# Optimization experiments

Measured on AMD Instinct MI355X. Metric: run time of the kernel, lower is better.

Reference implementation:

```python
import jax, jax.numpy as jnp
import numpy as np

N, E = 25000, 400000
IN, HID, OUT = 128, 256, 128
T = 4                      # towers
F1, F2 = HID // T, OUT // T  # per-tower out dims (divide_input=False)
A = 12                     # len(aggregators)=4 * len(scalers)=3
EPS_STD = 1e-5
EPS_BN = 1e-5


def _glorot(k, shape):
    fin, fout = shape[-2], shape[-1]
    lim = float(np.sqrt(6.0 / (fin + fout)))
    return jax.random.uniform(k, shape, jnp.float32, -lim, lim)


def setup_inputs():
    key = jax.random.key(0)
    ks = jax.random.split(key, 10)
    x = jax.random.normal(ks[0], (N, IN), jnp.float32)
    edge_index = jax.random.randint(ks[1], (2, E), 0, N, dtype=jnp.int32)
    # avg_deg['log'] buffer of PNAConv: mean over nodes of log(deg+1)
    deg = jax.ops.segment_sum(jnp.ones((E,), jnp.float32), edge_index[1], num_segments=N)
    avg_log = jnp.mean(jnp.log(deg + 1.0)).astype(jnp.float32)
    return dict(
        x=x, edge_index=edge_index, avg_log=avg_log,
        pre1_W=_glorot(ks[2], (T, 2 * IN, F1)), pre1_b=jnp.zeros((T, F1), jnp.float32),
        post1_W=_glorot(ks[3], (T, IN + A * F1, F1)), post1_b=jnp.zeros((T, F1), jnp.float32),
        lin1_W=_glorot(ks[4], (T * F1, HID)), lin1_b=jnp.zeros((HID,), jnp.float32),
        bn1_g=jnp.ones((HID,), jnp.float32), bn1_b=jnp.zeros((HID,), jnp.float32),
        pre2_W=_glorot(ks[5], (T, 2 * HID, F2)), pre2_b=jnp.zeros((T, F2), jnp.float32),
        post2_W=_glorot(ks[6], (T, HID + A * F2, F2)), post2_b=jnp.zeros((T, F2), jnp.float32),
        lin2_W=_glorot(ks[7], (T * F2, OUT)), lin2_b=jnp.zeros((OUT,), jnp.float32),
        bn2_g=jnp.ones((OUT,), jnp.float32), bn2_b=jnp.zeros((OUT,), jnp.float32),
    )


def _pna(x, src, tgt, preW, preB, postW, postB, linW, linB, avg_log):
    """PNAConv: towers=T, divide_input=False, pre_layers=post_layers=1,
    aggregators [mean,min,max,std], scalers [identity,amplification,attenuation]."""
    n = x.shape[0]
    # message: per tower Linear on concat([x_i, x_j]) where i=target, j=source
    h = jnp.concatenate([x[tgt], x[src]], axis=-1)            # [E, 2*F_in]
    msg = jnp.einsum('ec,tcf->etf', h, preW) + preB           # [E, T, F]
    ones = jnp.ones((msg.shape[0],), msg.dtype)
    deg = jax.ops.segment_sum(ones, tgt, num_segments=n)      # in-degree [n]
    degc = jnp.maximum(deg, 1.0)[:, None, None]
    s1 = jax.ops.segment_sum(msg, tgt, num_segments=n)
    mean = s1 / degc
    s2 = jax.ops.segment_sum(msg * msg, tgt, num_segments=n)
    var = jnp.maximum(s2 / degc - mean * mean, 0.0)
    std = jnp.sqrt(var + EPS_STD)
    has = (deg > 0.0)[:, None, None]
    mn = jnp.where(has, jax.ops.segment_min(msg, tgt, num_segments=n), 0.0)
    mx = jnp.where(has, jax.ops.segment_max(msg, tgt, num_segments=n), 0.0)
    agg = jnp.concatenate([mean, mn, mx, std], axis=-1)       # [n, T, 4F]
    dlog = jnp.log(jnp.maximum(deg, 1.0) + 1.0)[:, None, None]
    out = jnp.concatenate([agg, agg * (dlog / avg_log), agg * (avg_log / dlog)], axis=-1)  # [n, T, 12F]
    xt = jnp.broadcast_to(x[:, None, :], (n, T, x.shape[-1]))
    post_in = jnp.concatenate([xt, out], axis=-1)             # [n, T, F_in + 12F]
    post = jnp.einsum('ntc,tcf->ntf', post_in, postW) + postB # [n, T, F]
    return post.reshape(n, -1) @ linW + linB                  # [n, out]


def _bn(x, g, b):
    # BatchNorm1d training-mode math: biased batch variance
    m = jnp.mean(x, axis=0)
    v = jnp.mean((x - m) ** 2, axis=0)
    return g * (x - m) / jnp.sqrt(v + EPS_BN) + b


def reference(x, edge_index, avg_log, pre1_W, pre1_b, post1_W, post1_b, lin1_W, lin1_b,
              bn1_g, bn1_b, pre2_W, pre2_b, post2_W, post2_b, lin2_W, lin2_b, bn2_g, bn2_b):
    src, tgt = edge_index[0], edge_index[1]
    h = _pna(x, src, tgt, pre1_W, pre1_b, post1_W, post1_b, lin1_W, lin1_b, avg_log)
    h = jax.nn.relu(_bn(jnp.nan_to_num(h), bn1_g, bn1_b))
    h = _pna(h, src, tgt, pre2_W, pre2_b, post2_W, post2_b, lin2_W, lin2_b, avg_log)
    h = jax.nn.relu(_bn(jnp.nan_to_num(h), bn2_g, bn2_b))
    return h
```

## Files before the change

kernel.cpp:

```cpp
#include <hip/hip_runtime.h>
#include <hip/hip_bf16.h>
#include <float.h>
#include <math.h>

typedef __hip_bfloat16 bf16;
typedef __attribute__((ext_vector_type(8))) short short8;
typedef __attribute__((ext_vector_type(4))) float f32x4;

__device__ __forceinline__ float bf2f(bf16 v){ return __bfloat162float(v); }
__device__ __forceinline__ void stv(float* p, float v){ *p = v; }
__device__ __forceinline__ void stv(bf16* p, float v){ *p = __float2bfloat16(v); }
__device__ __forceinline__ float nanfix(float v){
  if (v != v) return 0.f;
  return fminf(fmaxf(v, -FLT_MAX), FLT_MAX);
}
__device__ __forceinline__ unsigned short f2bu(float f){
  unsigned u = __float_as_uint(f);
  unsigned r = u + 0x7FFFu + ((u>>16)&1u);
  return (unsigned short)(r>>16);
}
template<int VEC>
__device__ __forceinline__ void ldbf(const bf16* p, float (&o)[VEC]){
  if constexpr (VEC==4){
    ushort4 r = *(const ushort4*)p;
    o[0]=__uint_as_float((unsigned)r.x<<16); o[1]=__uint_as_float((unsigned)r.y<<16);
    o[2]=__uint_as_float((unsigned)r.z<<16); o[3]=__uint_as_float((unsigned)r.w<<16);
  } else {
    ushort2 r = *(const ushort2*)p;
    o[0]=__uint_as_float((unsigned)r.x<<16); o[1]=__uint_as_float((unsigned)r.y<<16);
  }
}

__device__ __forceinline__ void gl_lds16(const bf16* g, bf16* l){
  __builtin_amdgcn_global_load_lds(
      (const __attribute__((address_space(1))) void*)g,
      (__attribute__((address_space(3))) void*)l, 16, 0, 0);
}

__global__ void k_scan1(const int* __restrict__ deg, int* __restrict__ bsum, int N){
  __shared__ int sm[256];
  int i = blockIdx.x*256 + threadIdx.x;
  sm[threadIdx.x] = (i < N) ? deg[i] : 0;
  __syncthreads();
  for (int off = 128; off > 0; off >>= 1){
    if (threadIdx.x < off) sm[threadIdx.x] += sm[threadIdx.x + off];
    __syncthreads();
  }
  if (threadIdx.x == 0) bsum[blockIdx.x] = sm[0];
}

__global__ void k_scan2(int* __restrict__ bsum, int NB){
  __shared__ int sm[1024];
  int tid = threadIdx.x;
  sm[tid] = (tid < NB) ? bsum[tid] : 0;
  __syncthreads();
  for (int off = 1; off < 1024; off <<= 1){
    int t = (tid >= off) ? sm[tid-off] : 0;
    __syncthreads();
    sm[tid] += t;
    __syncthreads();
  }
  if (tid < NB) bsum[tid] = (tid == 0) ? 0 : sm[tid-1];
}

__global__ void k_scan3(const int* __restrict__ deg, const int* __restrict__ bsum,
                        int* __restrict__ offs, int N){
  __shared__ int sm[256];
  int tid = threadIdx.x;
  int i = blockIdx.x*256 + tid;
  int v = (i < N) ? deg[i] : 0;
  sm[tid] = v; __syncthreads();
  for (int off = 1; off < 256; off <<= 1){
    int t = (tid >= off) ? sm[tid-off] : 0;
    __syncthreads();
    sm[tid] += t;
    __syncthreads();
  }
  if (i < N) offs[i+1] = bsum[blockIdx.x] + sm[tid];
  if (i == 0) offs[0] = 0;
}

__global__ void k_scatter(const int* __restrict__ src, const int* __restrict__ tgt,
                          const int* __restrict__ offs, int* __restrict__ cnt,
                          int* __restrict__ ssrc, int E){
  int e = blockIdx.x*blockDim.x + threadIdx.x;
  if (e < E){
    int t = tgt[e];
    int pos = offs[t] + atomicAdd(&cnt[t], 1);
    ssrc[pos] = src[e];
  }
}

__device__ __forceinline__ void rp_pqT(const float* preW, const float* preB,
                                       bf16* WpqT, float* bpq, int K, int F, int idx){
  int NC = 4*F;
  int total = 2*NC*K;
  if (idx < total){
    int j = idx/K, c = idx%K;
    int half = j/NC, jj = j%NC, t = jj/F, f = jj%F;
    WpqT[idx] = __float2bfloat16(preW[(t*2*K + half*K + c)*F + f]);
  }
  if (idx < 2*NC) bpq[idx] = (idx < NC) ? preB[idx] : 0.f;
}
__device__ __forceinline__ void rp_xT(const float* postW, const float* postB,
                                      bf16* WxT, float* bpost, int KX, int F, int idx){
  int NC = 4*F; int KP = KX + 12*F;
  if (idx < NC*KX){
    int j = idx/KX, c = idx%KX, t = j/F, f = j%F;
    WxT[idx] = __float2bfloat16(postW[(t*KP + c)*F + f]);
  }
  if (idx < NC) bpost[idx] = postB[idx];
}
__device__ __forceinline__ void rp_agg3(const float* postW, bf16* Wagg3,
                                        int KX, int F, int idx){
  int K4F = 4*F; int KP = KX + 12*F;
  int total = 4*3*F*K4F;
  if (idx < total){
    int k = idx % K4F; int r = idx / K4F;
    int zr = r % (3*F); int t = r / (3*F);
    int s = zr / F, f = zr % F;
    Wagg3[idx] = __float2bfloat16(postW[((size_t)(t*KP + KX + s*K4F + k))*F + f]);
  }
}
__device__ __forceinline__ void rp_linT(const float* linW, bf16* WlinT,
                                        int K, int NC, int idx){
  if (idx < NC*K){
    int j = idx/K, c = idx%K;
    WlinT[idx] = __float2bfloat16(linW[c*NC + j]);
  }
}

struct SetupArgs {
  const float *pre1W, *pre1b, *post1W, *post1b, *lin1W;
  const float *pre2W, *pre2b, *post2W, *post2b, *lin2W;
  const float *x;
  const int *tgt;
  bf16 *WpqT1, *WxT1, *Wagg31, *lin1WT;
  bf16 *WpqT2, *WxT2, *Wagg32, *lin2WT;
  bf16 *x_bf;
  int *deg;
  float *bpq1, *bpost1, *bpq2, *bpost2;
  int nx4;
  int E;
  int gstride;
};

__global__ void k_setup(SetupArgs a){
  int idx = blockIdx.x*256 + threadIdx.x;
  switch (blockIdx.y){
    case 0: rp_pqT (a.pre1W, a.pre1b, a.WpqT1, a.bpq1, 128, 64, idx); break;
    case 1: rp_xT  (a.post1W, a.post1b, a.WxT1, a.bpost1, 128, 64, idx); break;
    case 2: rp_agg3(a.post1W, a.Wagg31, 128, 64, idx); break;
    case 3: rp_linT(a.lin1W, a.lin1WT, 256, 256, idx); break;
    case 4: rp_pqT (a.pre2W, a.pre2b, a.WpqT2, a.bpq2, 256, 32, idx); break;
    case 5: rp_xT  (a.post2W, a.post2b, a.WxT2, a.bpost2, 256, 32, idx); break;
    case 6: rp_agg3(a.post2W, a.Wagg32, 256, 32, idx); break;
    case 7: rp_linT(a.lin2W, a.lin2WT, 128, 128, idx); break;
    case 8:
      for (int i = idx; i < a.nx4; i += a.gstride){
        float4 v = *(const float4*)(a.x + (size_t)i*4);
        ushort4 o = make_ushort4(f2bu(v.x), f2bu(v.y), f2bu(v.z), f2bu(v.w));
        *(ushort4*)(a.x_bf + (size_t)i*4) = o;
      }
      break;
    case 9:
      for (int e = idx; e < a.E; e += a.gstride)
        atomicAdd(&a.deg[a.tgt[e]], 1);
      break;
  }
}

template<typename TO, bool STATS>
__global__ __launch_bounds__(256) void k_mgemm(
    const bf16* __restrict__ A, int lda,
    const bf16* __restrict__ Bt,
    const float* __restrict__ bias,
    TO* __restrict__ Cout, int ldc,
    int N, int K, int NC, float* __restrict__ part)
{
  __shared__ __align__(16) bf16 As[2][64*32];
  __shared__ __align__(16) bf16 Bs[2][64*32];
  __shared__ float sstat[4][2][16][2];
  int n0 = blockIdx.y*64;
  int j0 = blockIdx.x*64;
  int tid = threadIdx.x;
  int srow = tid>>2, skoff = (tid&3)*8;
  int wave = tid>>6, lane = tid&63;
  int wy = (wave>>1)*32, wx = (wave&1)*32;
  int l15 = lane&15, q = lane>>4;
  f32x4 acc[2][2] = {};
  const bf16* Ag = A  + (size_t)(n0 + srow)*lda + skoff;
  const bf16* Bg = Bt + (size_t)(j0 + srow)*K   + skoff;
  int nt = K >> 5;
  gl_lds16(Ag, &As[0][tid*8]);
  gl_lds16(Bg, &Bs[0][tid*8]);
  __syncthreads();
  for (int t = 0; t < nt; t++){
    int cur = t & 1;
    if (t + 1 < nt){
      gl_lds16(Ag + (t+1)*32, &As[cur^1][tid*8]);
      gl_lds16(Bg + (t+1)*32, &Bs[cur^1][tid*8]);
    }
    short8 af[2], bfr[2];
    #pragma unroll
    for (int i = 0; i < 2; i++){
      af[i]  = *(const short8*)&As[cur][(wy + i*16 + l15)*32 + q*8];
      bfr[i] = *(const short8*)&Bs[cur][(wx + i*16 + l15)*32 + q*8];
    }
    #pragma unroll
    for (int mi = 0; mi < 2; mi++)
      #pragma unroll
      for (int ni = 0; ni < 2; ni++)
        acc[mi][ni] = __builtin_amdgcn_mfma_f32_16x16x32_bf16(af[mi], bfr[ni], acc[mi][ni], 0, 0, 0);
    __syncthreads();
  }
  float cs[2] = {0.f, 0.f}, cq[2] = {0.f, 0.f};
  #pragma unroll
  for (int mi = 0; mi < 2; mi++){
    #pragma unroll
    for (int ni = 0; ni < 2; ni++){
      #pragma unroll
      for (int r = 0; r < 4; r++){
        int n  = n0 + wy + mi*16 + q*4 + r;
        int jj = j0 + wx + ni*16 + l15;
        if (n < N && jj < NC){
          float v = acc[mi][ni][r] + bias[jj];
          stv(&Cout[(size_t)n*ldc + jj], v);
          if constexpr (STATS){ cs[ni] += v; cq[ni] = fmaf(v, v, cq[ni]); }
        }
      }
    }
  }
  if constexpr (STATS){
    #pragma unroll
    for (int ni = 0; ni < 2; ni++){
      float s = cs[ni], qq = cq[ni];
      s  += __shfl_xor(s, 16);  s  += __shfl_xor(s, 32);
      qq += __shfl_xor(qq, 16); qq += __shfl_xor(qq, 32);
      if (q == 0){ sstat[wave][ni][l15][0] = s; sstat[wave][ni][l15][1] = qq; }
    }
    __syncthreads();
    if (tid < 64){
      int j = tid;
      int wa = (j < 32) ? 0 : 1, wb = wa + 2;
      int ni = (j & 31) >> 4, li = j & 15;
      float s  = sstat[wa][ni][li][0] + sstat[wb][ni][li][0];
      float qq = sstat[wa][ni][li][1] + sstat[wb][ni][li][1];
      part[(size_t)blockIdx.y*2*ldc + (j0 + j)]       = s;
      part[(size_t)blockIdx.y*2*ldc + ldc + (j0 + j)] = qq;
    }
  }
}

template<int COLS>
__global__ __launch_bounds__(256) void k_postagg(
    const bf16* __restrict__ agg,
    const bf16* __restrict__ Wagg3,
    const bf16* __restrict__ PQX, int ldq, int cinOff,
    const float* __restrict__ scal,
    bf16* __restrict__ Cout, int ldc, int N)
{
  constexpr int K4F = 4*COLS;
  constexpr int ROWS3 = 3*COLS;
  constexpr int NI = COLS/32;
  constexpr int LDA_AGG = 16*COLS;
  constexpr int BROW3 = (ROWS3 + 63)/64;
  __shared__ __align__(16) bf16 As[2][128*32];
  __shared__ __align__(16) bf16 Bs[2][ROWS3*32];
  int z = blockIdx.z;
  int n0 = blockIdx.y*128;
  int tid = threadIdx.x;
  int srow = tid>>2, skoff = (tid&3)*8;
  int wave = tid>>6, lane = tid&63;
  int wy = (wave>>1)*64;
  int wx = (wave&1)*(COLS/2);
  int l15 = lane&15, q = lane>>4;
  f32x4 acc[4][NI][3] = {};
  const bf16* Ag = agg + (size_t)z*K4F + (size_t)(n0 + srow)*LDA_AGG + skoff;
  const bf16* Bg = Wagg3 + (size_t)z*ROWS3*K4F + (size_t)srow*K4F + skoff;
  constexpr int NT = K4F/32;
  gl_lds16(Ag,                          &As[0][srow*32 + skoff]);
  gl_lds16(Ag + (size_t)64*LDA_AGG,     &As[0][(srow+64)*32 + skoff]);
  #pragma unroll
  for (int r = 0; r < BROW3; r++){
    int rr = srow + r*64;
    if (ROWS3 % 64 == 0 || rr < ROWS3)
      gl_lds16(Bg + (size_t)r*64*K4F, &Bs[0][rr*32 + skoff]);
  }
  __syncthreads();
  for (int t = 0; t < NT; t++){
    int cur = t & 1;
    if (t + 1 < NT){
      gl_lds16(Ag + (t+1)*32,                      &As[cur^1][srow*32 + skoff]);
      gl_lds16(Ag + (t+1)*32 + (size_t)64*LDA_AGG, &As[cur^1][(srow+64)*32 + skoff]);
      #pragma unroll
      for (int r = 0; r < BROW3; r++){
        int rr = srow + r*64;
        if (ROWS3 % 64 == 0 || rr < ROWS3)
          gl_lds16(Bg + (size_t)r*64*K4F + (t+1)*32, &Bs[cur^1][rr*32 + skoff]);
      }
    }
    short8 af[4];
    #pragma unroll
    for (int i = 0; i < 4; i++)
      af[i] = *(const short8*)&As[cur][(wy + i*16 + l15)*32 + q*8];
    #pragma unroll
    for (int s = 0; s < 3; s++){
      #pragma unroll
      for (int ni = 0; ni < NI; ni++){
        short8 bfr = *(const short8*)&Bs[cur][(s*COLS + wx + ni*16 + l15)*32 + q*8];
        #pragma unroll
        for (int mi = 0; mi < 4; mi++)
          acc[mi][ni][s] = __builtin_amdgcn_mfma_f32_16x16x32_bf16(af[mi], bfr, acc[mi][ni][s], 0, 0, 0);
      }
    }
    __syncthreads();
  }
  #pragma unroll
  for (int mi = 0; mi < 4; mi++){
    #pragma unroll
    for (int ni = 0; ni < NI; ni++){
      int jj = wx + ni*16 + l15;
      int jg = z*COLS + jj;
      #pragma unroll
      for (int r = 0; r < 4; r++){
        int n = n0 + wy + mi*16 + q*4 + r;
        if (n < N){
          float s1 = scal[2*n], s2 = scal[2*n+1];
          float cin = bf2f(PQX[(size_t)n*ldq + cinOff + jg]);
          float v = cin + acc[mi][ni][0][r] + s1*acc[mi][ni][1][r] + s2*acc[mi][ni][2][r];
          Cout[(size_t)n*ldc + jg] = __float2bfloat16(v);
        }
      }
    }
  }
}

template<int NC, int F, int LDA>
__global__ __launch_bounds__(256) void k_agg(const bf16* __restrict__ PQ,
    const int* __restrict__ ssrc, const int* __restrict__ offs,
    const float* __restrict__ avgp,
    bf16* __restrict__ agg, float* __restrict__ scal, int N)
{
  constexpr int VEC = NC/64;
  int lane = threadIdx.x & 63;
  int n = __builtin_amdgcn_readfirstlane((int)(blockIdx.x*4 + (threadIdx.x>>6)));
  if (n >= N) return;
  int c0 = lane*VEC;
  float p[VEC];
  ldbf<VEC>(PQ + (size_t)n*LDA + c0, p);
  int s0 = __builtin_amdgcn_readfirstlane(offs[n]);
  int s1 = __builtin_amdgcn_readfirstlane(offs[n+1]);
  int deg = s1 - s0;
  float sum[VEC], sq[VEC], mn[VEC], mx[VEC];
  #pragma unroll
  for (int v=0;v<VEC;v++){ sum[v]=0.f; sq[v]=0.f; mn[v]=FLT_MAX; mx[v]=-FLT_MAX; }
  const bf16* Q = PQ + NC + c0;
  if (deg > 0){
    int last = s1 - 1;
    int se[8];
    #pragma unroll
    for (int u=0;u<8;u++) se[u] = ssrc[min(s0+u, last)];
    for (int i = s0; i < s1; i += 8){
      int sn[8];
      bool more = (i + 8 < s1);
      if (more){
        #pragma unroll
        for (int u=0;u<8;u++) sn[u] = ssrc[min(i+8+u, last)];
      }
      float qv[8][VEC];
      #pragma unroll
      for (int u=0;u<8;u++) ldbf<VEC>(Q + (size_t)se[u]*LDA, qv[u]);
      int rem = s1 - i;
      if (rem >= 8){
        #pragma unroll
        for (int u=0;u<8;u++){
          #pragma unroll
          for (int v=0;v<VEC;v++){
            float qq = qv[u][v];
            sum[v] += qq; sq[v] = fmaf(qq,qq,sq[v]);
            mn[v] = fminf(mn[v],qq); mx[v] = fmaxf(mx[v],qq);
          }
        }
      } else {
        #pragma unroll
        for (int u=0;u<8;u++){
          bool valid = u < rem;
          #pragma unroll
          for (int v=0;v<VEC;v++){
            float qq = qv[u][v];
            float tq = valid ? qq : 0.f;
            sum[v] += tq; sq[v] = fmaf(tq,qq,sq[v]);
            mn[v] = fminf(mn[v],qq); mx[v] = fmaxf(mx[v],qq);
          }
        }
      }
      if (more){
        #pragma unroll
        for (int u=0;u<8;u++) se[u] = sn[u];
      }
    }
  }
  float degf = (float)deg;
  float degc = fmaxf(degf, 1.f);
  float rdeg = 1.f/degc;
  unsigned short um[VEC], un[VEC], ux[VEC], us[VEC];
  #pragma unroll
  for (int v=0;v<VEC;v++){
    float pv = p[v];
    float sum_m = fmaf(degf, pv, sum[v]);
    float sq_m  = sq[v] + 2.f*pv*sum[v] + degf*pv*pv;
    float mean = sum_m*rdeg;
    float var = fmaxf(fmaf(sq_m, rdeg, -mean*mean), 0.f);
    float sd = sqrtf(var + 1e-5f);
    float mnv = deg>0 ? pv + mn[v] : 0.f;
    float mxv = deg>0 ? pv + mx[v] : 0.f;
    um[v]=f2bu(mean); un[v]=f2bu(mnv); ux[v]=f2bu(mxv); us[v]=f2bu(sd);
  }
  int t = c0 / F, f0 = c0 % F;
  bf16* base = agg + (size_t)n*4*NC + (size_t)t*4*F + f0;
  if constexpr (VEC==4){
    *(ushort4*)(base)       = make_ushort4(um[0],um[1],um[2],um[3]);
    *(ushort4*)(base + F)   = make_ushort4(un[0],un[1],un[2],un[3]);
    *(ushort4*)(base + 2*F) = make_ushort4(ux[0],ux[1],ux[2],ux[3]);
    *(ushort4*)(base + 3*F) = make_ushort4(us[0],us[1],us[2],us[3]);
  } else {
    *(ushort2*)(base)       = make_ushort2(um[0],um[1]);
    *(ushort2*)(base + F)   = make_ushort2(un[0],un[1]);
    *(ushort2*)(base + 2*F) = make_ushort2(ux[0],ux[1]);
    *(ushort2*)(base + 3*F) = make_ushort2(us[0],us[1]);
  }
  if (lane == 0){
    float dlog = logf(degc + 1.f);
    float avg = *avgp;
    scal[2*n]   = dlog/avg;
    scal[2*n+1] = avg/dlog;
  }
}

template<int C>
__global__ __launch_bounds__(256) void k_bn_final(const float* __restrict__ part, int PB,
                                                  float* __restrict__ stats){
  int c = blockIdx.x*256 + threadIdx.x;
  if (c >= 2*C) return;
  int CH = gridDim.y;
  int per = (PB + CH - 1)/CH;
  int p0 = blockIdx.y*per, p1 = min(p0 + per, PB);
  float acc = 0.f;
  int p = p0;
  for (; p+4 <= p1; p += 4){
    acc += part[(size_t)p*2*C + c] + part[(size_t)(p+1)*2*C + c]
         + part[(size_t)(p+2)*2*C + c] + part[(size_t)(p+3)*2*C + c];
  }
  for (; p < p1; p++) acc += part[(size_t)p*2*C + c];
  atomicAdd(&stats[c], acc);
}

template<typename TO, int C>
__global__ void k_bn_apply(const bf16* __restrict__ h, const float* __restrict__ stats,
     const float* __restrict__ g, const float* __restrict__ b,
     TO* __restrict__ out, int N){
  int idx = blockIdx.x*blockDim.x + threadIdx.x;
  if (idx >= N*(C/4)) return;
  int c = (idx % (C/4))*4;
  float fn = (float)N;
  float v[4];
  ldbf<4>(h + (size_t)idx*4, v);
  float r[4];
  #pragma unroll
  for (int k = 0; k < 4; k++){
    float m = stats[c+k]/fn;
    float var = fmaxf(stats[C+c+k]/fn - m*m, 0.f);
    float inv = rsqrtf(var + 1e-5f);
    float vv = nanfix(v[k]);
    r[k] = fmaxf(g[c+k]*(vv - m)*inv + b[c+k], 0.f);
  }
  if constexpr (sizeof(TO) == 4){
    float4 o = {r[0], r[1], r[2], r[3]};
    *(float4*)((float*)out + (size_t)idx*4) = o;
  } else {
    ushort4 o = make_ushort4(f2bu(r[0]), f2bu(r[1]), f2bu(r[2]), f2bu(r[3]));
    *(ushort4*)((bf16*)out + (size_t)idx*4) = o;
  }
}

static inline int cdiv(int a, int b){ return (a + b - 1)/b; }

extern "C" void kernel_launch(void* const* d_in, const int* in_sizes, int n_in,
                              void* d_out, int out_size, void* d_ws, size_t ws_size,
                              hipStream_t stream){
  const int IN = 128, HID = 256, T = 4, F1 = 64, F2 = 32;
  const int N = in_sizes[0]/IN;
  const int E = in_sizes[1]/2;
  const int NC1 = T*F1;
  const int NC2 = T*F2;
  const int LDQ1 = 2*NC1 + NC1;
  const int LDQ2 = 2*NC2 + NC2;

  const float* x      = (const float*)d_in[0];
  const int*   ei     = (const int*)  d_in[1];
  const int*   srcE   = ei;
  const int*   tgtE   = ei + E;
  const float* avgp   = (const float*)d_in[2];
  const float* pre1W  = (const float*)d_in[3];
  const float* pre1b  = (const float*)d_in[4];
  const float* post1W = (const float*)d_in[5];
  const float* post1b = (const float*)d_in[6];
  const float* lin1W  = (const float*)d_in[7];
  const float* lin1b  = (const float*)d_in[8];
  const float* bn1g   = (const float*)d_in[9];
  const float* bn1b   = (const float*)d_in[10];
  const float* pre2W  = (const float*)d_in[11];
  const float* pre2b  = (const float*)d_in[12];
  const float* post2W = (const float*)d_in[13];
  const float* post2b = (const float*)d_in[14];
  const float* lin2W  = (const float*)d_in[15];
  const float* lin2b  = (const float*)d_in[16];
  const float* bn2g   = (const float*)d_in[17];
  const float* bn2b   = (const float*)d_in[18];

  char* w = (char*)d_ws;
  auto alloc = [&](size_t bytes)->void*{
    void* p = (void*)w; w += (bytes + 255) & ~(size_t)255; return p;
  };
  bf16* BT1    = (bf16*)alloc((size_t)LDQ1*IN*2);
  bf16* WpqT1  = BT1;              bf16* WxT1 = BT1 + (size_t)2*NC1*IN;
  float* bias1 = (float*)alloc((size_t)LDQ1*4);
  float* bpq1  = bias1;            float* bpost1 = bias1 + 2*NC1;
  bf16* Wagg31 = (bf16*)alloc((size_t)T*3*F1*4*F1*2);
  bf16* lin1WT = (bf16*)alloc((size_t)HID*NC1*2);
  bf16* BT2    = (bf16*)alloc((size_t)LDQ2*HID*2);
  bf16* WpqT2  = BT2;              bf16* WxT2 = BT2 + (size_t)2*NC2*HID;
  float* bias2 = (float*)alloc((size_t)LDQ2*4);
  float* bpq2  = bias2;            float* bpost2 = bias2 + 2*NC2;
  bf16* Wagg32 = (bf16*)alloc((size_t)T*3*F2*4*F2*2);
  bf16* lin2WT = (bf16*)alloc((size_t)128*NC2*2);
  int* deg_i   = (int*)alloc((size_t)N*4);
  int* cnt     = (int*)alloc((size_t)N*4);
  float* stats = (float*)alloc(1024*4);
  size_t zbytes = (size_t)((char*)stats - (char*)deg_i) + 1024*4;
  int* offs    = (int*)alloc((size_t)(N+1)*4);
  int* bsum    = (int*)alloc((size_t)cdiv(N,256)*4);
  int* ssrc    = (int*)alloc((size_t)E*4);
  bf16* x_bf   = (bf16*)alloc((size_t)N*IN*2);
  bf16* PQX    = (bf16*)alloc((size_t)N*LDQ1*2);
  bf16* aggb   = (bf16*)alloc((size_t)N*4*NC1*2);
  float* scal  = (float*)alloc((size_t)N*2*4);
  bf16* postbb = (bf16*)alloc((size_t)N*256*2);
  bf16* hpre   = (bf16*)alloc((size_t)N*256*2);
  bf16* h1b    = (bf16*)alloc((size_t)N*256*2);
  int NB = cdiv(N,64);
  int NB128 = cdiv(N,128);
  float* part  = (float*)alloc((size_t)NB*512*4);

  hipMemsetAsync(deg_i, 0, zbytes, stream);

  int sgx = cdiv(T*3*F1*4*F1, 256);
  SetupArgs sa = { pre1W, pre1b, post1W, post1b, lin1W,
                   pre2W, pre2b, post2W, post2b, lin2W,
                   x, tgtE,
                   WpqT1, WxT1, Wagg31, lin1WT,
                   WpqT2, WxT2, Wagg32, lin2WT,
                   x_bf, deg_i,
                   bpq1, bpost1, bpq2, bpost2,
                   N*IN/4, E, sgx*256 };
  k_setup<<<dim3(sgx, 10),256,0,stream>>>(sa);

  int NBs = cdiv(N,256);
  k_scan1<<<NBs,256,0,stream>>>(deg_i, bsum, N);
  k_scan2<<<1,1024,0,stream>>>(bsum, NBs);
  k_scan3<<<NBs,256,0,stream>>>(deg_i, bsum, offs, N);
  k_scatter<<<cdiv(E,256),256,0,stream>>>(srcE, tgtE, offs, cnt, ssrc, E);

  k_mgemm<bf16,false><<<dim3(LDQ1/64,NB),256,0,stream>>>(x_bf, IN, BT1, bias1, PQX, LDQ1, N, IN, LDQ1, nullptr);
  k_agg<256,64,768><<<cdiv(N,4),256,0,stream>>>(PQX, ssrc, offs, avgp, aggb, scal, N);
  k_postagg<64><<<dim3(1,NB128,T),256,0,stream>>>(aggb, Wagg31, PQX, LDQ1, 2*NC1, scal,
                                                  postbb, NC1, N);
  k_mgemm<bf16,true><<<dim3(4,NB),256,0,stream>>>(postbb, NC1, lin1WT, lin1b, hpre, HID, N, NC1, HID, part);
  k_bn_final<256><<<dim3(2,4),256,0,stream>>>(part, NB, stats);
  k_bn_apply<bf16,256><<<cdiv(N*64,256),256,0,stream>>>(hpre, stats, bn1g, bn1b, h1b, N);

  k_mgemm<bf16,false><<<dim3(LDQ2/64,NB),256,0,stream>>>(h1b, HID, BT2, bias2, PQX, LDQ2, N, HID, LDQ2, nullptr);
  k_agg<128,32,384><<<cdiv(N,4),256,0,stream>>>(PQX, ssrc, offs, avgp, aggb, scal, N);
  k_postagg<32><<<dim3(1,NB128,T),256,0,stream>>>(aggb, Wagg32, PQX, LDQ2, 2*NC2, scal,
                                                  postbb, NC2, N);
  k_mgemm<bf16,true><<<dim3(2,NB),256,0,stream>>>(postbb, NC2, lin2WT, lin2b, hpre, 128, N, NC2, 128, part);
  k_bn_final<128><<<dim3(1,4),256,0,stream>>>(part, NB, stats + 512);
  k_bn_apply<float,128><<<cdiv(N*32,256),256,0,stream>>>(hpre, stats + 512, bn2g, bn2b, (float*)d_out, N);
}
```

Baseline: 364.2 us.

## Remap GEMM blocks across XCDs, fuse BN stats via atomics, split agg loop

Three changes. The mgemm kernel remaps block indices so consecutive tiles land on the same XCD, for better L2 locality. The BN partial-sum buffer and the k_bn_final reduction kernel are replaced by direct float atomicAdds into the stats array from each GEMM block. This removes two launches but adds atomic contention on 512 addresses and a nondeterministic summation order. The aggregation loop is split into full groups of 8 and a separate tail pass, which removes the per-iteration min-clamp and remainder branch.

```diff
diff --git a/kernel.cpp b/kernel.cpp
--- a/kernel.cpp
+++ b/kernel.cpp
@@ -35,6 +35,15 @@
   __builtin_amdgcn_global_load_lds(
       (const __attribute__((address_space(1))) void*)g,
       (__attribute__((address_space(3))) void*)l, 16, 0, 0);
+}
+
+__device__ __forceinline__ void xcd_remap(int gx, int total, int &bx, int &by){
+  int orig = by*gx + bx;
+  int q8 = total >> 3, r8 = total & 7;
+  int xcd = orig & 7, rest = orig >> 3;
+  int nid = (xcd < r8) ? (xcd*(q8+1) + rest)
+                       : (r8*(q8+1) + (xcd-r8)*q8 + rest);
+  bx = nid % gx; by = nid / gx;
 }
 
 __global__ void k_scan1(const int* __restrict__ deg, int* __restrict__ bsum, int N){
@@ -176,13 +185,15 @@
     const bf16* __restrict__ Bt,
     const float* __restrict__ bias,
     TO* __restrict__ Cout, int ldc,
-    int N, int K, int NC, float* __restrict__ part)
+    int N, int K, int NC, float* __restrict__ stats)
 {
   __shared__ __align__(16) bf16 As[2][64*32];
   __shared__ __align__(16) bf16 Bs[2][64*32];
   __shared__ float sstat[4][2][16][2];
-  int n0 = blockIdx.y*64;
-  int j0 = blockIdx.x*64;
+  int bx = blockIdx.x, by = blockIdx.y;
+  xcd_remap(gridDim.x, gridDim.x*gridDim.y, bx, by);
+  int n0 = by*64;
+  int j0 = bx*64;
   int tid = threadIdx.x;
   int srow = tid>>2, skoff = (tid&3)*8;
   int wave = tid>>6, lane = tid&63;
@@ -246,8 +257,8 @@
       int ni = (j & 31) >> 4, li = j & 15;
       float s  = sstat[wa][ni][li][0] + sstat[wb][ni][li][0];
       float qq = sstat[wa][ni][li][1] + sstat[wb][ni][li][1];
-      part[(size_t)blockIdx.y*2*ldc + (j0 + j)]       = s;
-      part[(size_t)blockIdx.y*2*ldc + ldc + (j0 + j)] = qq;
+      atomicAdd(&stats[j0 + j], s);
+      atomicAdd(&stats[ldc + j0 + j], qq);
     }
   }
 }
@@ -358,46 +369,58 @@
   const bf16* Q = PQ + NC + c0;
   if (deg > 0){
     int last = s1 - 1;
-    int se[8];
-    #pragma unroll
-    for (int u=0;u<8;u++) se[u] = ssrc[min(s0+u, last)];
-    for (int i = s0; i < s1; i += 8){
-      int sn[8];
-      bool more = (i + 8 < s1);
-      if (more){
+    int nfull = deg >> 3;
+    int tail  = deg & 7;
+    int se[8], sn[8];
+    if (nfull > 0){
+      #pragma unroll
+      for (int u=0;u<8;u++) se[u] = ssrc[s0+u];
+    } else {
+      #pragma unroll
+      for (int u=0;u<8;u++) se[u] = ssrc[min(s0+u, last)];
+    }
+    for (int g = 0; g < nfull; g++){
+      bool moref = (g + 1 < nfull);
+      bool tailn = (g + 1 == nfull) && (tail != 0);
+      int base = s0 + (g+1)*8;
+      if (moref){
         #pragma unroll
-        for (int u=0;u<8;u++) sn[u] = ssrc[min(i+8+u, last)];
+        for (int u=0;u<8;u++) sn[u] = ssrc[base+u];
+      } else if (tailn){
+        #pragma unroll
+        for (int u=0;u<8;u++) sn[u] = ssrc[min(base+u, last)];
       }
       float qv[8][VEC];
       #pragma unroll
       for (int u=0;u<8;u++) ldbf<VEC>(Q + (size_t)se[u]*LDA, qv[u]);
-      int rem = s1 - i;
-      if (rem >= 8){
+      #pragma unroll
+      for (int u=0;u<8;u++){
         #pragma unroll
-        for (int u=0;u<8;u++){
-          #pragma unroll
-          for (int v=0;v<VEC;v++){
-            float qq = qv[u][v];
-            sum[v] += qq; sq[v] = fmaf(qq,qq,sq[v]);
-            mn[v] = fminf(mn[v],qq); mx[v] = fmaxf(mx[v],qq);
-          }
+        for (int v=0;v<VEC;v++){
+          float qq = qv[u][v];
+          sum[v] += qq; sq[v] = fmaf(qq,qq,sq[v]);
+          mn[v] = fminf(mn[v],qq); mx[v] = fmaxf(mx[v],qq);
         }
-      } else {
-        #pragma unroll
-        for (int u=0;u<8;u++){
-          bool valid = u < rem;
-          #pragma unroll
-          for (int v=0;v<VEC;v++){
-            float qq = qv[u][v];
-            float tq = valid ? qq : 0.f;
-            sum[v] += tq; sq[v] = fmaf(tq,qq,sq[v]);
-            mn[v] = fminf(mn[v],qq); mx[v] = fmaxf(mx[v],qq);
-          }
-        }
-      }
-      if (more){
+      }
+      if (moref || tailn){
         #pragma unroll
         for (int u=0;u<8;u++) se[u] = sn[u];
+      }
+    }
+    if (tail){
+      float qv[8][VEC];
+      #pragma unroll
+      for (int u=0;u<8;u++) ldbf<VEC>(Q + (size_t)se[u]*LDA, qv[u]);
+      #pragma unroll
+      for (int u=0;u<8;u++){
+        bool valid = u < tail;
+        #pragma unroll
+        for (int v=0;v<VEC;v++){
+          float qq = qv[u][v];
+          float tq = valid ? qq : 0.f;
+          sum[v] += tq; sq[v] = fmaf(tq,qq,sq[v]);
+          mn[v] = fminf(mn[v],qq); mx[v] = fmaxf(mx[v],qq);
+        }
       }
     }
   }
@@ -436,24 +459,6 @@
     scal[2*n]   = dlog/avg;
     scal[2*n+1] = avg/dlog;
   }
-}
-
-template<int C>
-__global__ __launch_bounds__(256) void k_bn_final(const float* __restrict__ part, int PB,
-                                                  float* __restrict__ stats){
-  int c = blockIdx.x*256 + threadIdx.x;
-  if (c >= 2*C) return;
-  int CH = gridDim.y;
-  int per = (PB + CH - 1)/CH;
-  int p0 = blockIdx.y*per, p1 = min(p0 + per, PB);
-  float acc = 0.f;
-  int p = p0;
-  for (; p+4 <= p1; p += 4){
-    acc += part[(size_t)p*2*C + c] + part[(size_t)(p+1)*2*C + c]
-         + part[(size_t)(p+2)*2*C + c] + part[(size_t)(p+3)*2*C + c];
-  }
-  for (; p < p1; p++) acc += part[(size_t)p*2*C + c];
-  atomicAdd(&stats[c], acc);
 }
 
 template<typename TO, int C>
@@ -551,7 +556,6 @@
   bf16* h1b    = (bf16*)alloc((size_t)N*256*2);
   int NB = cdiv(N,64);
   int NB128 = cdiv(N,128);
-  float* part  = (float*)alloc((size_t)NB*512*4);
 
   hipMemsetAsync(deg_i, 0, zbytes, stream);
 
@@ -576,15 +580,13 @@
   k_agg<256,64,768><<<cdiv(N,4),256,0,stream>>>(PQX, ssrc, offs, avgp, aggb, scal, N);
   k_postagg<64><<<dim3(1,NB128,T),256,0,stream>>>(aggb, Wagg31, PQX, LDQ1, 2*NC1, scal,
                                                   postbb, NC1, N);
-  k_mgemm<bf16,true><<<dim3(4,NB),256,0,stream>>>(postbb, NC1, lin1WT, lin1b, hpre, HID, N, NC1, HID, part);
-  k_bn_final<256><<<dim3(2,4),256,0,stream>>>(part, NB, stats);
+  k_mgemm<bf16,true><<<dim3(4,NB),256,0,stream>>>(postbb, NC1, lin1WT, lin1b, hpre, HID, N, NC1, HID, stats);
   k_bn_apply<bf16,256><<<cdiv(N*64,256),256,0,stream>>>(hpre, stats, bn1g, bn1b, h1b, N);
 
   k_mgemm<bf16,false><<<dim3(LDQ2/64,NB),256,0,stream>>>(h1b, HID, BT2, bias2, PQX, LDQ2, N, HID, LDQ2, nullptr);
   k_agg<128,32,384><<<cdiv(N,4),256,0,stream>>>(PQX, ssrc, offs, avgp, aggb, scal, N);
   k_postagg<32><<<dim3(1,NB128,T),256,0,stream>>>(aggb, Wagg32, PQX, LDQ2, 2*NC2, scal,
                                                   postbb, NC2, N);
-  k_mgemm<bf16,true><<<dim3(2,NB),256,0,stream>>>(postbb, NC2, lin2WT, lin2b, hpre, 128, N, NC2, 128, part);
-  k_bn_final<128><<<dim3(1,4),256,0,stream>>>(part, NB, stats + 512);
+  k_mgemm<bf16,true><<<dim3(2,NB),256,0,stream>>>(postbb, NC2, lin2WT, lin2b, hpre, 128, N, NC2, 128, stats + 512);
   k_bn_apply<float,128><<<cdiv(N*32,256),256,0,stream>>>(hpre, stats + 512, bn2g, bn2b, (float*)d_out, N);
 }
```

Result: faster. 351.1 us (-3.6%).
